# Optimization experiments

Measured on AMD Instinct MI355X. Metric: run time of the kernel, lower is better.

Reference implementation:

```python
import jax, jax.numpy as jnp
import numpy as np

N, E, H, L, G = 50000, 800000, 128, 4, 64

def setup_inputs() -> dict:
    key = jax.random.key(0)
    ks = jax.random.split(key, 16)
    s = 0.05
    x = jax.random.normal(ks[0], (N, H), jnp.float32)
    edge_index = jax.random.randint(ks[1], (2, E), 0, N)
    edge_attr = jax.random.normal(ks[2], (E, 1), jnp.float32)
    # sorted graph assignment covering all G graphs (batch[-1]+1 == G)
    batch = (jnp.arange(N) * G) // N
    conv_W1 = jax.random.normal(ks[3], (L, H, H), jnp.float32) * s
    conv_b1 = jnp.zeros((L, H), jnp.float32)
    conv_W2 = jax.random.normal(ks[4], (L, H, H), jnp.float32) * s
    conv_b2 = jnp.zeros((L, H), jnp.float32)
    conv_eps = jnp.zeros((L,), jnp.float32)  # torch init: eps = 0
    edge_W = jax.random.normal(ks[5], (L, 1, H), jnp.float32) * s
    edge_b = jnp.zeros((L, H), jnp.float32)
    vn_W1 = jax.random.normal(ks[6], (L - 1, H, H), jnp.float32) * s
    vn_b1 = jnp.zeros((L - 1, H), jnp.float32)
    vn_W2 = jax.random.normal(ks[7], (L - 1, H, H), jnp.float32) * s
    vn_b2 = jnp.zeros((L - 1, H), jnp.float32)
    vn_emb = jnp.zeros((H,), jnp.float32)  # torch init: constant 0
    return dict(x=x, edge_attr=edge_attr, conv_W1=conv_W1, conv_b1=conv_b1,
                conv_W2=conv_W2, conv_b2=conv_b2, conv_eps=conv_eps,
                edge_W=edge_W, edge_b=edge_b, vn_W1=vn_W1, vn_b1=vn_b1,
                vn_W2=vn_W2, vn_b2=vn_b2, vn_emb=vn_emb,
                edge_index=edge_index, batch=batch)


def reference(x, edge_attr, conv_W1, conv_b1, conv_W2, conv_b2, conv_eps,
              edge_W, edge_b, vn_W1, vn_b1, vn_W2, vn_b2, vn_emb,
              edge_index, batch):
    src, tgt = edge_index[0], edge_index[1]
    # PyG mean aggregation: divide scatter-sum by in-degree (clamped to 1)
    deg = jnp.maximum(
        jax.ops.segment_sum(jnp.ones((E,), x.dtype), tgt, num_segments=N), 1.0)[:, None]
    vn = jnp.broadcast_to(vn_emb[None, :], (G, H))  # virtual node per graph
    h = x
    hs = []
    for i in range(L):
        h = h + vn[batch]
        edge_emb = edge_attr @ edge_W[i] + edge_b[i]          # [E,H]
        msg = jax.nn.relu(h[src] + edge_emb)                   # gather + relu
        agg = jax.ops.segment_sum(msg, tgt, num_segments=N) / deg  # mean scatter
        z = (1.0 + conv_eps[i]) * h + agg
        h = jax.nn.relu(z @ conv_W1[i] + conv_b1[i]) @ conv_W2[i] + conv_b2[i]
        hs.append(h)
        if i < L - 1:
            vt = jax.ops.segment_sum(hs[i], batch, num_segments=G) + vn
            vn = jax.nn.relu(
                jax.nn.relu(vt @ vn_W1[i] + vn_b1[i]) @ vn_W2[i] + vn_b2[i])
            # eval mode: dropout is identity
    return jnp.concatenate(hs, axis=1)  # [N, L*H] jumping-knowledge concat
```

## Files before the change

kernel.cpp:

```cpp
#include <hip/hip_runtime.h>

#define NN 50000
#define EE 800000
#define HH 128
#define LL 4
#define GG 64
#define NR 50048
#define NS 8

typedef short bf16x8 __attribute__((ext_vector_type(8)));
typedef float f32x4 __attribute__((ext_vector_type(4)));

__device__ __forceinline__ unsigned bf_round(float f) {
  unsigned u = __float_as_uint(f);
  return (u + 0x7fffu + ((u >> 16) & 1u)) >> 16;
}
__device__ __forceinline__ unsigned bf_pack2(float lo, float hi) {
  return bf_round(lo) | (bf_round(hi) << 16);
}

__global__ __launch_bounds__(256) void count_init_pack0_kernel(
    const int* __restrict__ tgt, int* __restrict__ cnt, int E, int nbE, int initB,
    const float* __restrict__ W1, const float* __restrict__ W2,
    const float* __restrict__ emb, short* __restrict__ wt1, short* __restrict__ wt2,
    float* __restrict__ vnA, float* __restrict__ part01,
    const float4* __restrict__ x4, const float* __restrict__ eb0,
    uint2* __restrict__ hbf, int N) {
  int bid = blockIdx.x;
  int t = threadIdx.x;
  if (bid < nbE) {
    int e = bid * 256 + t;
    if (e < E) atomicAdd(&cnt[tgt[e]], 1);
    return;
  }
  if (bid < nbE + initB) {
    int idx = (bid - nbE) * 256 + t;
    const int NW = 2 * LL * HH * HH;
    if (idx < NW) {
      int m = idx >> 14;
      int r = idx & 16383;
      int n = r >> 7, k = r & 127;
      const float* W = (m < LL) ? (W1 + (size_t)m * 16384) : (W2 + (size_t)(m - LL) * 16384);
      short* D = (m < LL) ? (wt1 + (size_t)m * 16384) : (wt2 + (size_t)(m - LL) * 16384);
      D[n * 128 + k] = (short)bf_round(W[k * 128 + n]);
    } else if (idx < NW + GG * HH) {
      int i = idx - NW;
      vnA[i] = emb[i & (HH - 1)];
    } else if (idx < NW + 3 * GG * HH) {
      part01[idx - NW - GG * HH] = 0.f;
    }
    return;
  }
  int pidx = (bid - nbE - initB) * 256 + t;
  if (pidx >= N * (HH / 4)) return;
  int c4 = pidx & 31;
  float4 a = x4[pidx];
  const float4 v = *(const float4*)(emb + c4 * 4);
  const float4 e = *(const float4*)(eb0 + c4 * 4);
  uint2 o;
  o.x = bf_pack2(a.x + v.x + e.x, a.y + v.y + e.y);
  o.y = bf_pack2(a.z + v.z + e.z, a.w + v.w + e.w);
  hbf[pidx] = o;
}

__global__ __launch_bounds__(256) void rp_scan_kernel(const int* __restrict__ cnt,
                                                      int* __restrict__ rp,
                                                      int* __restrict__ cur, int N, int nb) {
  int b = blockIdx.x, t = threadIdx.x;
  int i = b * 256 + t;
  int pre = 0;
  for (int j = t; j < b * 256; j += 256) pre += cnt[j];
  __shared__ int sm[256];
  sm[t] = pre;
  __syncthreads();
  for (int s = 128; s >= 1; s >>= 1) {
    if (t < s) sm[t] += sm[t + s];
    __syncthreads();
  }
  int prefix = sm[0];
  __syncthreads();
  int v = (i < N) ? cnt[i] : 0;
  sm[t] = v;
  __syncthreads();
  for (int off = 1; off < 256; off <<= 1) {
    int u = (t >= off) ? sm[t - off] : 0;
    __syncthreads();
    sm[t] += u;
    __syncthreads();
  }
  if (i < N) { rp[i] = prefix + sm[t] - v; cur[i] = 0; }
  if (b == nb - 1 && t == 255) rp[N] = prefix + sm[255];
}

__global__ __launch_bounds__(256) void scatter_kernel(const int* __restrict__ src,
                                                      const int* __restrict__ tgt,
                                                      const float* __restrict__ attr,
                                                      const int* __restrict__ rp,
                                                      int* __restrict__ cur,
                                                      int2* __restrict__ es, int E) {
  int e = blockIdx.x * 256 + threadIdx.x;
  if (e < E) {
    int t = tgt[e];
    int p = rp[t] + atomicAdd(&cur[t], 1);
    int2 rec;
    rec.x = src[e];
    rec.y = __float_as_int(attr[e]);
    es[p] = rec;
  }
}

__device__ __forceinline__ void accum8s(float* acc, uint4 p, float a, float m,
                                        const float4& ew0, const float4& ew1) {
  acc[0] = fmaf(m, fmaxf(fmaf(a, ew0.x, __uint_as_float(p.x << 16)), 0.f), acc[0]);
  acc[1] = fmaf(m, fmaxf(fmaf(a, ew0.y, __uint_as_float(p.x & 0xffff0000u)), 0.f), acc[1]);
  acc[2] = fmaf(m, fmaxf(fmaf(a, ew0.z, __uint_as_float(p.y << 16)), 0.f), acc[2]);
  acc[3] = fmaf(m, fmaxf(fmaf(a, ew0.w, __uint_as_float(p.y & 0xffff0000u)), 0.f), acc[3]);
  acc[4] = fmaf(m, fmaxf(fmaf(a, ew1.x, __uint_as_float(p.z << 16)), 0.f), acc[4]);
  acc[5] = fmaf(m, fmaxf(fmaf(a, ew1.y, __uint_as_float(p.z & 0xffff0000u)), 0.f), acc[5]);
  acc[6] = fmaf(m, fmaxf(fmaf(a, ew1.z, __uint_as_float(p.w << 16)), 0.f), acc[6]);
  acc[7] = fmaf(m, fmaxf(fmaf(a, ew1.w, __uint_as_float(p.w & 0xffff0000u)), 0.f), acc[7]);
}

__global__ __launch_bounds__(128) void agg_kernel(const uint4* __restrict__ hbf4,
                                                  const float* __restrict__ hp, int pitch,
                                                  const float* __restrict__ vnp,
                                                  const int* __restrict__ batch,
                                                  const int2* __restrict__ es,
                                                  const int* __restrict__ rp,
                                                  const float* __restrict__ eW,
                                                  const float* __restrict__ epsp,
                                                  uint4* __restrict__ zb4, int N) {
  int wave = threadIdx.x >> 6;
  int lane = threadIdx.x & 63;
  int n = blockIdx.x * 2 + wave;
  if (n >= N) return;
  int q = lane >> 4;
  int c = lane & 15;
  float4 ew0 = *(const float4*)(eW + c * 8);
  float4 ew1 = *(const float4*)(eW + c * 8 + 4);
  int rs = rp[n], re = rp[n + 1];
  int cnt = re - rs;
  float acc[8];
#pragma unroll
  for (int j = 0; j < 8; ++j) acc[j] = 0.f;
  for (int k = 0; k < cnt; k += 16) {
    int i0 = rs + min(k + q, cnt - 1);
    int i1 = rs + min(k + 4 + q, cnt - 1);
    int i2 = rs + min(k + 8 + q, cnt - 1);
    int i3 = rs + min(k + 12 + q, cnt - 1);
    int2 e0 = es[i0];
    int2 e1 = es[i1];
    int2 e2 = es[i2];
    int2 e3 = es[i3];
    uint4 p0 = hbf4[(size_t)e0.x * 16 + c];
    uint4 p1 = hbf4[(size_t)e1.x * 16 + c];
    uint4 p2 = hbf4[(size_t)e2.x * 16 + c];
    uint4 p3 = hbf4[(size_t)e3.x * 16 + c];
    float m0 = (k + q < cnt) ? 1.f : 0.f;
    float m1 = (k + 4 + q < cnt) ? 1.f : 0.f;
    float m2 = (k + 8 + q < cnt) ? 1.f : 0.f;
    float m3 = (k + 12 + q < cnt) ? 1.f : 0.f;
    accum8s(acc, p0, __int_as_float(e0.y), m0, ew0, ew1);
    accum8s(acc, p1, __int_as_float(e1.y), m1, ew0, ew1);
    accum8s(acc, p2, __int_as_float(e2.y), m2, ew0, ew1);
    accum8s(acc, p3, __int_as_float(e3.y), m3, ew0, ew1);
  }
#pragma unroll
  for (int j = 0; j < 8; ++j) {
    acc[j] += __shfl_xor(acc[j], 16);
    acc[j] += __shfl_xor(acc[j], 32);
  }
  int g = batch[n];
  const float* hrow = hp + (size_t)n * pitch + c * 8;
  const float* vrow = vnp + g * HH + c * 8;
  float4 h0 = *(const float4*)(hrow);
  float4 h1 = *(const float4*)(hrow + 4);
  float4 v0 = *(const float4*)(vrow);
  float4 v1 = *(const float4*)(vrow + 4);
  float inv = 1.f / fmaxf((float)cnt, 1.f);
  float onep = 1.f + epsp[0];
  uint4 o;
  o.x = bf_pack2(fmaf(onep, h0.x + v0.x, acc[0] * inv),
                 fmaf(onep, h0.y + v0.y, acc[1] * inv));
  o.y = bf_pack2(fmaf(onep, h0.z + v0.z, acc[2] * inv),
                 fmaf(onep, h0.w + v0.w, acc[3] * inv));
  o.z = bf_pack2(fmaf(onep, h1.x + v1.x, acc[4] * inv),
                 fmaf(onep, h1.y + v1.y, acc[5] * inv));
  o.w = bf_pack2(fmaf(onep, h1.z + v1.z, acc[6] * inv),
                 fmaf(onep, h1.w + v1.w, acc[7] * inv));
  if (q == 0) zb4[(size_t)n * 16 + c] = o;
}

__global__ __launch_bounds__(256) void mlp_kernel(const unsigned* __restrict__ zb,
                                                  const short* __restrict__ wt1,
                                                  const float* __restrict__ b1,
                                                  const short* __restrict__ wt2,
                                                  const float* __restrict__ b2,
                                                  float* __restrict__ out,
                                                  float* __restrict__ part,
                                                  int do_gs, int layer, int N) {
  __shared__ char smem[64 * 272];
  int tid = threadIdx.x;
  int w = tid >> 6, lane = tid & 63;
  int l15 = lane & 15, q = lane >> 4;
  int row0 = blockIdx.x * 64;
  int wrow = w * 16;

  const uint4* z4 = (const uint4*)zb;
#pragma unroll
  for (int it = 0; it < 4; ++it) {
    int f = lane + it * 64;
    int r = f >> 4, c16 = f & 15;
    uint4 v = z4[(size_t)(row0 + wrow + r) * 16 + c16];
    *(uint4*)(&smem[(wrow + r) * 272 + c16 * 16]) = v;
  }

  f32x4 zero = {0.f, 0.f, 0.f, 0.f};
  f32x4 acc[8];
#pragma unroll
  for (int j = 0; j < 8; ++j) acc[j] = zero;

#pragma unroll
  for (int s = 0; s < 4; ++s) {
    bf16x8 af = *(const bf16x8*)(&smem[(wrow + l15) * 272 + (s * 32 + q * 8) * 2]);
#pragma unroll
    for (int j = 0; j < 8; ++j) {
      bf16x8 bf = *(const bf16x8*)(wt1 + (size_t)(j * 16 + l15) * 128 + s * 32 + q * 8);
      acc[j] = __builtin_amdgcn_mfma_f32_16x16x32_bf16(af, bf, acc[j], 0, 0, 0);
    }
  }
#pragma unroll
  for (int j = 0; j < 8; ++j) {
    float bv = b1[j * 16 + l15];
#pragma unroll
    for (int r = 0; r < 4; ++r) {
      float v = fmaxf(acc[j][r] + bv, 0.f);
      *(short*)(&smem[(wrow + q * 4 + r) * 272 + (j * 16 + l15) * 2]) = (short)bf_round(v);
    }
    acc[j] = zero;
  }
#pragma unroll
  for (int s = 0; s < 4; ++s) {
    bf16x8 af = *(const bf16x8*)(&smem[(wrow + l15) * 272 + (s * 32 + q * 8) * 2]);
#pragma unroll
    for (int j = 0; j < 8; ++j) {
      bf16x8 bf = *(const bf16x8*)(wt2 + (size_t)(j * 16 + l15) * 128 + s * 32 + q * 8);
      acc[j] = __builtin_amdgcn_mfma_f32_16x16x32_bf16(af, bf, acc[j], 0, 0, 0);
    }
  }
  int g0 = (int)(((long long)row0 * GG) / NN);
#pragma unroll
  for (int j = 0; j < 8; ++j) {
    float bv = b2[j * 16 + l15];
    float s0 = 0.f, s1 = 0.f;
#pragma unroll
    for (int r = 0; r < 4; ++r) {
      int row = row0 + wrow + q * 4 + r;
      if (row < N) {
        float v = acc[j][r] + bv;
        out[(size_t)row * (LL * HH) + layer * HH + j * 16 + l15] = v;
        if (do_gs) {
          int rel = (int)(((long long)row * GG) / NN) - g0;
          if (rel == 0) s0 += v; else s1 += v;
        }
      }
    }
    if (do_gs) {
      s0 += __shfl_xor(s0, 16); s0 += __shfl_xor(s0, 32);
      s1 += __shfl_xor(s1, 16); s1 += __shfl_xor(s1, 32);
      if (q == 0) {
        atomicAdd(&part[g0 * HH + j * 16 + l15], s0);
        if (s1 != 0.f) atomicAdd(&part[(g0 + 1) * HH + j * 16 + l15], s1);
      }
    }
  }
}

__global__ __launch_bounds__(256) void vnpack_kernel(const float* __restrict__ part_in,
                                                     float* __restrict__ part_zero,
                                                     const float* __restrict__ vn_in,
                                                     float* __restrict__ vn_out,
                                                     const float* __restrict__ W1,
                                                     const float* __restrict__ b1,
                                                     const float* __restrict__ W2,
                                                     const float* __restrict__ b2,
                                                     const float* __restrict__ outp,
                                                     const float* __restrict__ ebn,
                                                     uint2* __restrict__ hbf,
                                                     int layer, int N) {
  int b = blockIdx.x;
  int g = b >> 3, s = b & (NS - 1);
  int t = threadIdx.x;
  __shared__ float vr[128];
  __shared__ float tr[128];
  __shared__ float vo[128];
  if (t < 128) vr[t] = vn_in[g * HH + t] + part_in[g * HH + t];
  __syncthreads();
  if (t < 128) {
    float a = b1[t];
    for (int k = 0; k < 128; ++k) a = fmaf(vr[k], W1[k * HH + t], a);
    tr[t] = fmaxf(a, 0.f);
  }
  __syncthreads();
  if (t < 128) {
    float o = b2[t];
    for (int k = 0; k < 128; ++k) o = fmaf(tr[k], W2[k * HH + t], o);
    float vn = fmaxf(o, 0.f);
    vo[t] = vn;
    if (s == 0) {
      vn_out[g * HH + t] = vn;
      part_zero[g * HH + t] = 0.f;
    }
  }
  __syncthreads();
  int r0 = (g * NN + GG - 1) / GG;
  int r1 = ((g + 1) * NN + GG - 1) / GG;
  if (r1 > N) r1 = N;
  int len = r1 - r0;
  int chunk = (len + NS - 1) / NS;
  int rs = r0 + s * chunk;
  int re = min(rs + chunk, r1);
  int c4 = t & 31;
  float4 v = *(const float4*)(vo + c4 * 4);
  float4 e = *(const float4*)(ebn + c4 * 4);
  const float4* o4 = (const float4*)outp;
  for (int n = rs + (t >> 5); n < re; n += 8) {
    float4 a = o4[(size_t)n * (LL * HH / 4) + layer * (HH / 4) + c4];
    uint2 o;
    o.x = bf_pack2(a.x + v.x + e.x, a.y + v.y + e.y);
    o.y = bf_pack2(a.z + v.z + e.z, a.w + v.w + e.w);
    hbf[(size_t)n * 32 + c4] = o;
  }
}

extern "C" void kernel_launch(void* const* d_in, const int* in_sizes, int n_in,
                              void* d_out, int out_size, void* d_ws, size_t ws_size,
                              hipStream_t stream) {
  const int N = NN, E = EE, H = HH, L = LL, G = GG;
  const float* x          = (const float*)d_in[0];
  const float* edge_attr  = (const float*)d_in[1];
  const float* conv_W1    = (const float*)d_in[2];
  const float* conv_b1    = (const float*)d_in[3];
  const float* conv_W2    = (const float*)d_in[4];
  const float* conv_b2    = (const float*)d_in[5];
  const float* conv_eps   = (const float*)d_in[6];
  const float* edge_W     = (const float*)d_in[7];
  const float* edge_b     = (const float*)d_in[8];
  const float* vn_W1      = (const float*)d_in[9];
  const float* vn_b1      = (const float*)d_in[10];
  const float* vn_W2      = (const float*)d_in[11];
  const float* vn_b2      = (const float*)d_in[12];
  const float* vn_emb     = (const float*)d_in[13];
  const int*   edge_index = (const int*)d_in[14];
  const int*   batch      = (const int*)d_in[15];
  float* out = (float*)d_out;

  const int nb = (N + 255) / 256;
  const int nbE = (E + 255) / 256;

  char* ws = (char*)d_ws;
  size_t off = 0;
  auto take = [&](size_t bytes) -> void* {
    void* p = ws + off;
    off = (off + bytes + 255) & ~(size_t)255;
    return p;
  };
  int*      cnt   = (int*)take((size_t)N * 4);
  int*      cur   = (int*)take((size_t)N * 4);
  int*      rp    = (int*)take((size_t)(N + 1) * 4);
  int2*     es    = (int2*)take((size_t)E * 8);
  unsigned* hbf   = (unsigned*)take((size_t)N * (H / 2) * 4);
  unsigned* zb    = (unsigned*)take((size_t)NR * (H / 2) * 4);
  short*    wt1   = (short*)take((size_t)L * H * H * 2);
  short*    wt2   = (short*)take((size_t)L * H * H * 2);
  float*    part  = (float*)take((size_t)2 * G * H * 4);
  float*    vnA   = (float*)take((size_t)G * H * 4);
  float*    vnB   = (float*)take((size_t)G * H * 4);

  const int* src = edge_index;
  const int* tgt = edge_index + E;

  hipMemsetAsync(cnt, 0, (size_t)N * 4, stream);
  const int initB = (2 * L * H * H + 3 * G * H + 255) / 256;
  const int packB = (N * (H / 4) + 255) / 256;
  count_init_pack0_kernel<<<nbE + initB + packB, 256, 0, stream>>>(
      tgt, cnt, E, nbE, initB, conv_W1, conv_W2, vn_emb, wt1, wt2, vnA, part,
      (const float4*)x, edge_b, (uint2*)hbf, N);
  rp_scan_kernel<<<nb, 256, 0, stream>>>(cnt, rp, cur, N, nb);
  scatter_kernel<<<nbE, 256, 0, stream>>>(src, tgt, edge_attr, rp, cur, es, E);

  for (int i = 0; i < L; ++i) {
    const float* hp;
    int pitch;
    if (i == 0) { hp = x; pitch = H; }
    else        { hp = out + (size_t)(i - 1) * H; pitch = L * H; }
    float* vin  = (i & 1) ? vnB : vnA;
    float* vout = (i & 1) ? vnA : vnB;
    agg_kernel<<<(N + 1) / 2, 128, 0, stream>>>(
        (const uint4*)hbf, hp, pitch, vin, batch, es, rp,
        edge_W + (size_t)i * H, conv_eps + i, (uint4*)zb, N);
    mlp_kernel<<<NR / 64, 256, 0, stream>>>(
        zb, wt1 + (size_t)i * H * H, conv_b1 + (size_t)i * H,
        wt2 + (size_t)i * H * H, conv_b2 + (size_t)i * H, out,
        part + (size_t)(i & 1) * G * H,
        (i < L - 1) ? 1 : 0, i, N);
    if (i < L - 1) {
      vnpack_kernel<<<G * NS, 256, 0, stream>>>(
          part + (size_t)(i & 1) * G * H,
          part + (size_t)((i + 1) & 1) * G * H,
          vin, vout,
          vn_W1 + (size_t)i * H * H, vn_b1 + (size_t)i * H,
          vn_W2 + (size_t)i * H * H, vn_b2 + (size_t)i * H,
          out, edge_b + (size_t)(i + 1) * H, (uint2*)hbf, i, N);
    }
  }
}
```

Baseline: 621.5 us.

## Split MLP block work across waves by output columns over 16 rows

```diff
diff --git a/kernel.cpp b/kernel.cpp
--- a/kernel.cpp
+++ b/kernel.cpp
@@ -199,65 +199,69 @@
                                                   float* __restrict__ out,
                                                   float* __restrict__ part,
                                                   int do_gs, int layer, int N) {
-  __shared__ char smem[64 * 272];
+  __shared__ char smem[2 * 16 * 272];
+  char* zr = smem;
+  char* rr = smem + 16 * 272;
   int tid = threadIdx.x;
   int w = tid >> 6, lane = tid & 63;
   int l15 = lane & 15, q = lane >> 4;
-  int row0 = blockIdx.x * 64;
-  int wrow = w * 16;
-
-  const uint4* z4 = (const uint4*)zb;
-#pragma unroll
-  for (int it = 0; it < 4; ++it) {
-    int f = lane + it * 64;
-    int r = f >> 4, c16 = f & 15;
-    uint4 v = z4[(size_t)(row0 + wrow + r) * 16 + c16];
-    *(uint4*)(&smem[(wrow + r) * 272 + c16 * 16]) = v;
-  }
+  int row0 = blockIdx.x * 16;
+
+  {
+    int r = w * 4 + q;
+    int c16 = l15;
+    uint4 v = ((const uint4*)zb)[(size_t)(row0 + r) * 16 + c16];
+    *(uint4*)(&zr[r * 272 + c16 * 16]) = v;
+  }
+  __syncthreads();
 
   f32x4 zero = {0.f, 0.f, 0.f, 0.f};
-  f32x4 acc[8];
-#pragma unroll
-  for (int j = 0; j < 8; ++j) acc[j] = zero;
+  f32x4 acc[2];
+  acc[0] = zero; acc[1] = zero;
 
 #pragma unroll
   for (int s = 0; s < 4; ++s) {
-    bf16x8 af = *(const bf16x8*)(&smem[(wrow + l15) * 272 + (s * 32 + q * 8) * 2]);
-#pragma unroll
-    for (int j = 0; j < 8; ++j) {
+    bf16x8 af = *(const bf16x8*)(&zr[l15 * 272 + (s * 32 + q * 8) * 2]);
+#pragma unroll
+    for (int jj = 0; jj < 2; ++jj) {
+      int j = w * 2 + jj;
       bf16x8 bf = *(const bf16x8*)(wt1 + (size_t)(j * 16 + l15) * 128 + s * 32 + q * 8);
-      acc[j] = __builtin_amdgcn_mfma_f32_16x16x32_bf16(af, bf, acc[j], 0, 0, 0);
-    }
-  }
-#pragma unroll
-  for (int j = 0; j < 8; ++j) {
+      acc[jj] = __builtin_amdgcn_mfma_f32_16x16x32_bf16(af, bf, acc[jj], 0, 0, 0);
+    }
+  }
+#pragma unroll
+  for (int jj = 0; jj < 2; ++jj) {
+    int j = w * 2 + jj;
     float bv = b1[j * 16 + l15];
 #pragma unroll
     for (int r = 0; r < 4; ++r) {
-      float v = fmaxf(acc[j][r] + bv, 0.f);
-      *(short*)(&smem[(wrow + q * 4 + r) * 272 + (j * 16 + l15) * 2]) = (short)bf_round(v);
-    }
-    acc[j] = zero;
-  }
+      float v = fmaxf(acc[jj][r] + bv, 0.f);
+      *(short*)(&rr[(q * 4 + r) * 272 + (j * 16 + l15) * 2]) = (short)bf_round(v);
+    }
+    acc[jj] = zero;
+  }
+  __syncthreads();
 #pragma unroll
   for (int s = 0; s < 4; ++s) {
-    bf16x8 af = *(const bf16x8*)(&smem[(wrow + l15) * 272 + (s * 32 + q * 8) * 2]);
-#pragma unroll
-    for (int j = 0; j < 8; ++j) {
+    bf16x8 af = *(const bf16x8*)(&rr[l15 * 272 + (s * 32 + q * 8) * 2]);
+#pragma unroll
+    for (int jj = 0; jj < 2; ++jj) {
+      int j = w * 2 + jj;
       bf16x8 bf = *(const bf16x8*)(wt2 + (size_t)(j * 16 + l15) * 128 + s * 32 + q * 8);
-      acc[j] = __builtin_amdgcn_mfma_f32_16x16x32_bf16(af, bf, acc[j], 0, 0, 0);
+      acc[jj] = __builtin_amdgcn_mfma_f32_16x16x32_bf16(af, bf, acc[jj], 0, 0, 0);
     }
   }
   int g0 = (int)(((long long)row0 * GG) / NN);
 #pragma unroll
-  for (int j = 0; j < 8; ++j) {
+  for (int jj = 0; jj < 2; ++jj) {
+    int j = w * 2 + jj;
     float bv = b2[j * 16 + l15];
     float s0 = 0.f, s1 = 0.f;
 #pragma unroll
     for (int r = 0; r < 4; ++r) {
-      int row = row0 + wrow + q * 4 + r;
+      int row = row0 + q * 4 + r;
       if (row < N) {
-        float v = acc[j][r] + bv;
+        float v = acc[jj][r] + bv;
         out[(size_t)row * (LL * HH) + layer * HH + j * 16 + l15] = v;
         if (do_gs) {
           int rel = (int)(((long long)row * GG) / NN) - g0;
@@ -399,7 +403,7 @@
     agg_kernel<<<(N + 1) / 2, 128, 0, stream>>>(
         (const uint4*)hbf, hp, pitch, vin, batch, es, rp,
         edge_W + (size_t)i * H, conv_eps + i, (uint4*)zb, N);
-    mlp_kernel<<<NR / 64, 256, 0, stream>>>(
+    mlp_kernel<<<NR / 16, 256, 0, stream>>>(
         zb, wt1 + (size_t)i * H * H, conv_b1 + (size_t)i * H,
         wt2 + (size_t)i * H * H, conv_b2 + (size_t)i * H, out,
         part + (size_t)(i & 1) * G * H,
```

Result: faster. 583.5 us (-6.1%).
